# Kernel optimization log

Hardware: AMD Instinct MI355X
Metric: run time of the kernel (lower is better)

## Reference

```python
import jax, jax.numpy as jnp
import numpy as np

N = 100000
D = 128          # atom_input_dim
OUT = 256        # output_dim
HOPS = 3
E = 640000
IN_DIM = D * (HOPS + 1)  # 512


def setup_inputs() -> dict:
    key = jax.random.key(0)
    ks = jax.random.split(key, 16)
    s = 0.02
    inp = {
        "x": jax.random.normal(ks[0], (N, D), dtype=jnp.float32),
        "target": jax.random.randint(ks[1], (E,), 0, HOPS * N, dtype=jnp.int64),
        "src": jax.random.randint(ks[2], (E,), 0, HOPS * N, dtype=jnp.int64),
        "W_in": jax.random.normal(ks[3], (IN_DIM, OUT), dtype=jnp.float32) * s,
        "b_in": jnp.zeros((OUT,), dtype=jnp.float32),
        "W1_0": jax.random.normal(ks[4], (OUT, OUT), dtype=jnp.float32) * s,
        "b1_0": jnp.zeros((OUT,), dtype=jnp.float32),
        "W2_0": jax.random.normal(ks[5], (OUT, OUT), dtype=jnp.float32) * s,
        "b2_0": jnp.zeros((OUT,), dtype=jnp.float32),
        "W1_1": jax.random.normal(ks[6], (OUT, OUT), dtype=jnp.float32) * s,
        "b1_1": jnp.zeros((OUT,), dtype=jnp.float32),
        "W2_1": jax.random.normal(ks[7], (OUT, OUT), dtype=jnp.float32) * s,
        "b2_1": jnp.zeros((OUT,), dtype=jnp.float32),
        "W_skip": jax.random.normal(ks[8], (IN_DIM, OUT), dtype=jnp.float32) * s,
        "b_skip": jnp.zeros((OUT,), dtype=jnp.float32),
    }
    return inp


def reference(x, target, src, W_in, b_in, W1_0, b1_0, W2_0, b2_0,
              W1_1, b1_1, W2_1, b2_1, W_skip, b_skip):
    n = x.shape[0]
    # multi-hop message passing: tile node features HOPS times, gather by src,
    # scatter-add into target over the tiled index space [0, HOPS*n)
    expanded = jnp.tile(x, (HOPS, 1))                       # [HOPS*n, D]
    agg = jnp.zeros_like(expanded).at[target].add(expanded[src])
    # split per-hop chunks and concat with original features -> [n, (HOPS+1)*D]
    feats = jnp.concatenate([x] + [agg[h * n:(h + 1) * n] for h in range(HOPS)], axis=-1)
    h = jax.nn.silu(feats @ W_in + b_in)                    # [n, OUT]
    global_skip = feats @ W_skip + b_skip                   # input_dim != output_dim
    for W1, b1, W2, b2 in ((W1_0, b1_0, W2_0, b2_0), (W1_1, b1_1, W2_1, b2_1)):
        h = (jax.nn.silu(h @ W1 + b1)) @ W2 + b2 + h        # residual MLP block (dropout=0)
    return h + global_skip
```

## Files before the change

kernel.cpp:

```cpp
#include <hip/hip_runtime.h>
#include <math.h>

#define NN 100000
#define DD 128
#define OUT_DIM 256
#define HOPS 3
#define EDGES 640000
#define TGT (HOPS*NN)

typedef short bf16x8 __attribute__((ext_vector_type(8)));
typedef float f32x4 __attribute__((ext_vector_type(4)));

__device__ __forceinline__ unsigned short f2bf(float f) {
    unsigned u = __float_as_uint(f);
    unsigned r = u + 0x7FFFu + ((u >> 16) & 1u);
    return (unsigned short)(r >> 16);
}
__device__ __forceinline__ float bf2f(unsigned short s) {
    return __uint_as_float(((unsigned)s) << 16);
}
__device__ __forceinline__ float silu(float v) { return v / (1.0f + expf(-v)); }

__device__ __forceinline__ int swz(int c, int r) {
    return (c & ~63) | ((c & 63) ^ ((r & 7) << 3));
}

__device__ __forceinline__ void gload16(const unsigned short* g, unsigned short* l) {
    __builtin_amdgcn_global_load_lds(
        (const __attribute__((address_space(1))) void*)g,
        (__attribute__((address_space(3))) void*)l, 16, 0, 0);
}

__global__ __launch_bounds__(256) void k_hist(const int* __restrict__ tgt,
                                              int* __restrict__ cnt) {
    int e = blockIdx.x * 256 + threadIdx.x;
    atomicAdd(&cnt[tgt[e]], 1);
}

__global__ __launch_bounds__(512) void k_scanb(const int* __restrict__ cnt,
                                               int* __restrict__ off,
                                               int* __restrict__ part, int n) {
    __shared__ int s[512];
    int tid = threadIdx.x;
    int g = blockIdx.x * 512 + tid;
    int v = (g < n) ? cnt[g] : 0;
    s[tid] = v;
    __syncthreads();
    for (int d = 1; d < 512; d <<= 1) {
        int a = (tid >= d) ? s[tid - d] : 0;
        __syncthreads();
        s[tid] += a;
        __syncthreads();
    }
    if (g < n) off[g] = s[tid] - v;
    if (tid == 511) part[blockIdx.x] = s[511];
}

__global__ __launch_bounds__(1024) void k_scanp(int* __restrict__ part, int n) {
    __shared__ int s[1024];
    int t = threadIdx.x;
    s[t] = (t < n) ? part[t] : 0;
    __syncthreads();
    for (int d = 1; d < 1024; d <<= 1) {
        int a = (t >= d) ? s[t - d] : 0;
        __syncthreads();
        s[t] += a;
        __syncthreads();
    }
    if (t < n) part[t] = s[t];
}

__global__ __launch_bounds__(512) void k_addoff(int* __restrict__ off,
                                                const int* __restrict__ part,
                                                int* __restrict__ cursor, int n) {
    int g = blockIdx.x * 512 + threadIdx.x;
    if (g >= n) return;
    int add = (blockIdx.x > 0) ? part[blockIdx.x - 1] : 0;
    int o = off[g] + add;
    off[g] = o;
    cursor[g] = o;
}

__global__ __launch_bounds__(256) void k_fill(const int* __restrict__ tgt,
                                              const int* __restrict__ src,
                                              int* __restrict__ cursor,
                                              int* __restrict__ esrc) {
    int e = blockIdx.x * 256 + threadIdx.x;
    int t = tgt[e];
    int p = atomicAdd(&cursor[t], 1);
    esrc[p] = src[e] % NN;
}

__global__ __launch_bounds__(256) void k_aggfeats(const float* __restrict__ x,
                                                  const int* __restrict__ off,
                                                  const int* __restrict__ cur,
                                                  const int* __restrict__ esrc,
                                                  unsigned* __restrict__ feats) {
    int lane = threadIdx.x & 63;
    int r = blockIdx.x * 4 + (threadIdx.x >> 6);
    const float2* x2 = (const float2*)x;
    if (r < NN) {
        float2 v = x2[(size_t)r * 64 + lane];
        int p = lane;
        int ps = (p & ~31) | ((p & 31) ^ ((r & 7) << 2));
        feats[(size_t)r * 256 + ps] =
            (unsigned)f2bf(v.x) | ((unsigned)f2bf(v.y) << 16);
    } else {
        int t = r - NN;
        int hop = t / NN;
        int tn = t - hop * NN;
        int b = off[t], e = cur[t];
        float ax = 0.f, ay = 0.f;
        for (int i = b; i < e; ++i) {
            int sn = esrc[i];
            float2 v = x2[(size_t)sn * 64 + lane];
            ax += v.x; ay += v.y;
        }
        int p = 64 + hop * 64 + lane;
        int ps = (p & ~31) | ((p & 31) ^ ((tn & 7) << 2));
        feats[(size_t)tn * 256 + ps] =
            (unsigned)f2bf(ax) | ((unsigned)f2bf(ay) << 16);
    }
}

__global__ __launch_bounds__(256) void k_wprep(
    const float* __restrict__ Win, const float* __restrict__ Wskip,
    const float* __restrict__ W10, const float* __restrict__ W20,
    const float* __restrict__ W11, const float* __restrict__ W21,
    unsigned short* __restrict__ Wt1, unsigned short* __restrict__ Wt25) {
    int idx = blockIdx.x * 256 + threadIdx.x;
    if (idx < 262144) {
        int c = idx >> 9, k = idx & 511;
        int kl = swz(k, c);
        float v = (c < 256) ? Win[kl * 256 + c] : Wskip[kl * 256 + (c - 256)];
        Wt1[idx] = f2bf(v);
    } else {
        int j = idx - 262144;
        int m = j >> 16, rr = j & 65535;
        int c = rr >> 8, k = rr & 255;
        int kl = swz(k, c);
        const float* Wm = (m == 0) ? W10 : (m == 1) ? W20 : (m == 2) ? W11 : W21;
        Wt25[(size_t)m * 65536 + c * 256 + k] = f2bf(Wm[kl * 256 + c]);
    }
}

template <int K, int EPI>
__global__ __launch_bounds__(256) void k_gemm_t(
    const unsigned short* __restrict__ A, const unsigned short* __restrict__ Wt,
    const float* __restrict__ bias0, const float* __restrict__ bias1,
    const unsigned short* __restrict__ res1, const float* __restrict__ res2,
    unsigned short* __restrict__ Cb, float* __restrict__ Cf) {
    __shared__ unsigned short As[2][128 * 64];
    __shared__ unsigned short Bs[2][128 * 64];

    const int tid = threadIdx.x;
    const int lane = tid & 63;
    const int w = tid >> 6;
    const int row0 = blockIdx.x * 128;
    const int col0 = blockIdx.y * 128;

    const int wr = (w >> 1) * 64;
    const int wc = (w & 1) * 64;
    const int lr = lane & 15;
    const int lk8 = (lane >> 4) * 8;

    f32x4 acc[4][4];
    #pragma unroll
    for (int m = 0; m < 4; ++m)
        #pragma unroll
        for (int n = 0; n < 4; ++n) acc[m][n] = (f32x4){0.f, 0.f, 0.f, 0.f};

    const int NK = K / 64;

    auto STAGE = [&](int buf, int k0) {
        #pragma unroll
        for (int i = 0; i < 4; ++i) {
            int chunk = i * 4 + w;
            int slot = chunk * 64 + lane;
            int r = slot >> 3;
            int kq = (slot & 7) * 8;
            gload16(A + (size_t)(row0 + r) * K + k0 + kq, &As[buf][chunk * 512]);
            gload16(Wt + (size_t)(col0 + r) * K + k0 + kq, &Bs[buf][chunk * 512]);
        }
    };

    STAGE(0, 0);
    asm volatile("s_waitcnt vmcnt(0)" ::: "memory");
    __syncthreads();

    for (int ks = 0; ks < NK; ++ks) {
        int cur = ks & 1;
        if (ks + 1 < NK) STAGE(cur ^ 1, (ks + 1) * 64);

        #pragma unroll
        for (int ks2 = 0; ks2 < 2; ++ks2) {
            bf16x8 af[4], bfr[4];
            #pragma unroll
            for (int m = 0; m < 4; ++m) {
                int row = wr + m * 16 + lr;
                int eo = (ks2 * 32 + lk8) ^ ((row & 7) << 3);
                af[m] = *(const bf16x8*)&As[cur][row * 64 + eo];
            }
            #pragma unroll
            for (int n = 0; n < 4; ++n) {
                int row = wc + n * 16 + lr;
                int eo = (ks2 * 32 + lk8) ^ ((row & 7) << 3);
                bfr[n] = *(const bf16x8*)&Bs[cur][row * 64 + eo];
            }
            #pragma unroll
            for (int m = 0; m < 4; ++m)
                #pragma unroll
                for (int n = 0; n < 4; ++n)
                    acc[m][n] = __builtin_amdgcn_mfma_f32_16x16x32_bf16(
                        af[m], bfr[n], acc[m][n], 0, 0, 0);
        }
        asm volatile("s_waitcnt vmcnt(0)" ::: "memory");
        __syncthreads();
    }

    const int rq = (lane >> 4) * 4;
    #pragma unroll
    for (int m = 0; m < 4; ++m) {
        #pragma unroll
        for (int n = 0; n < 4; ++n) {
            int cg = col0 + wc + n * 16 + lr;
            float bb = (EPI == 3)
                           ? (cg < OUT_DIM ? bias0[cg] : bias1[cg - OUT_DIM])
                           : bias0[cg];
            #pragma unroll
            for (int j = 0; j < 4; ++j) {
                int r = row0 + wr + m * 16 + rq + j;
                if (r >= NN) continue;
                float v = acc[m][n][j] + bb;
                if (EPI == 3) {
                    if (cg < OUT_DIM)
                        Cb[(size_t)r * OUT_DIM + swz(cg, r)] = f2bf(silu(v));
                    else
                        Cf[(size_t)r * OUT_DIM + (cg - OUT_DIM)] = v;
                } else if (EPI == 0) {
                    Cb[(size_t)r * OUT_DIM + swz(cg, r)] = f2bf(silu(v));
                } else if (EPI == 1) {
                    size_t o = (size_t)r * OUT_DIM + swz(cg, r);
                    Cb[o] = f2bf(v + bf2f(res1[o]));
                } else {
                    size_t os = (size_t)r * OUT_DIM + swz(cg, r);
                    size_t ol = (size_t)r * OUT_DIM + cg;
                    Cf[ol] = v + bf2f(res1[os]) + res2[ol];
                }
            }
        }
    }
}

extern "C" void kernel_launch(void* const* d_in, const int* in_sizes, int n_in,
                              void* d_out, int out_size, void* d_ws, size_t ws_size,
                              hipStream_t stream) {
    const float* x      = (const float*)d_in[0];
    const int*   target = (const int*)d_in[1];
    const int*   src    = (const int*)d_in[2];
    const float* W_in   = (const float*)d_in[3];
    const float* b_in   = (const float*)d_in[4];
    const float* W1_0   = (const float*)d_in[5];
    const float* b1_0   = (const float*)d_in[6];
    const float* W2_0   = (const float*)d_in[7];
    const float* b2_0   = (const float*)d_in[8];
    const float* W1_1   = (const float*)d_in[9];
    const float* b1_1   = (const float*)d_in[10];
    const float* W2_1   = (const float*)d_in[11];
    const float* b2_1   = (const float*)d_in[12];
    const float* W_skip = (const float*)d_in[13];
    const float* b_skip = (const float*)d_in[14];
    float* out = (float*)d_out;

    char* p = (char*)d_ws;
    unsigned short* feats = (unsigned short*)p; p += (size_t)NN * 512 * 2;
    unsigned short* h0    = (unsigned short*)p; p += (size_t)NN * 256 * 2;
    unsigned short* h1    = (unsigned short*)p; p += (size_t)NN * 256 * 2;
    unsigned short* tb    = (unsigned short*)p; p += (size_t)NN * 256 * 2;
    unsigned short* Wt1   = (unsigned short*)p; p += 512 * 512 * 2;
    unsigned short* Wt25  = (unsigned short*)p; p += 4 * 256 * 256 * 2;
    int* cnt    = (int*)p; p += (size_t)TGT * 4;
    int* off    = (int*)p; p += (size_t)TGT * 4;
    int* cursor = (int*)p; p += (size_t)TGT * 4;
    int* esrc   = (int*)p; p += (size_t)EDGES * 4;
    int* part   = (int*)p; p += 4096;

    const int SCAN_BLOCKS = (TGT + 511) / 512;

    hipMemsetAsync(cnt, 0, (size_t)TGT * 4, stream);
    k_hist<<<EDGES / 256, 256, 0, stream>>>(target, cnt);
    k_scanb<<<SCAN_BLOCKS, 512, 0, stream>>>(cnt, off, part, TGT);
    k_scanp<<<1, 1024, 0, stream>>>(part, SCAN_BLOCKS);
    k_addoff<<<SCAN_BLOCKS, 512, 0, stream>>>(off, part, cursor, TGT);
    k_fill<<<EDGES / 256, 256, 0, stream>>>(target, src, cursor, esrc);

    k_aggfeats<<<NN, 256, 0, stream>>>(x, off, cursor, esrc, (unsigned*)feats);

    k_wprep<<<2048, 256, 0, stream>>>(W_in, W_skip, W1_0, W2_0, W1_1, W2_1,
                                      Wt1, Wt25);

    const int GM = (NN + 127) / 128;

    k_gemm_t<512, 3><<<dim3(GM, 4), 256, 0, stream>>>(
        feats, Wt1, b_in, b_skip, nullptr, nullptr, h0, out);

    k_gemm_t<256, 0><<<dim3(GM, 2), 256, 0, stream>>>(
        h0, Wt25 + 0 * 65536, b1_0, nullptr, nullptr, nullptr, tb, nullptr);
    k_gemm_t<256, 1><<<dim3(GM, 2), 256, 0, stream>>>(
        tb, Wt25 + 1 * 65536, b2_0, nullptr, h0, nullptr, h1, nullptr);

    k_gemm_t<256, 0><<<dim3(GM, 2), 256, 0, stream>>>(
        h1, Wt25 + 2 * 65536, b1_1, nullptr, nullptr, nullptr, tb, nullptr);
    k_gemm_t<256, 2><<<dim3(GM, 2), 256, 0, stream>>>(
        tb, Wt25 + 3 * 65536, b2_1, nullptr, h1, out, nullptr, out);
}
```

Baseline: 823.3 us.

## Fuse each residual MLP block into one kernel keeping hidden tile in LDS

Replaces the four separate GEMM launches for the two residual MLP blocks with two fused kernels. Each kernel loads a 128-row tile of h into LDS, computes silu(hW1+b1) into the same LDS buffer, then multiplies by W2 and adds the residual, so the intermediate never goes to global memory. The global skip is now stored in bf16 scratch instead of written as fp32 into the output and read back, which lowers skip precision. Blocks of 128 rows give only about 782 blocks of 512 threads and use large LDS, so occupancy may drop.

```diff
diff --git a/kernel.cpp b/kernel.cpp
--- a/kernel.cpp
+++ b/kernel.cpp
@@ -144,12 +144,11 @@
     }
 }
 
-template <int K, int EPI>
-__global__ __launch_bounds__(256) void k_gemm_t(
+__global__ __launch_bounds__(256) void k_gemm1(
     const unsigned short* __restrict__ A, const unsigned short* __restrict__ Wt,
     const float* __restrict__ bias0, const float* __restrict__ bias1,
-    const unsigned short* __restrict__ res1, const float* __restrict__ res2,
-    unsigned short* __restrict__ Cb, float* __restrict__ Cf) {
+    unsigned short* __restrict__ h0, unsigned short* __restrict__ gsk) {
+    const int K = 512;
     __shared__ unsigned short As[2][128 * 64];
     __shared__ unsigned short Bs[2][128 * 64];
 
@@ -169,8 +168,6 @@
     for (int m = 0; m < 4; ++m)
         #pragma unroll
         for (int n = 0; n < 4; ++n) acc[m][n] = (f32x4){0.f, 0.f, 0.f, 0.f};
-
-    const int NK = K / 64;
 
     auto STAGE = [&](int buf, int k0) {
         #pragma unroll
@@ -188,9 +185,9 @@
     asm volatile("s_waitcnt vmcnt(0)" ::: "memory");
     __syncthreads();
 
-    for (int ks = 0; ks < NK; ++ks) {
+    for (int ks = 0; ks < 8; ++ks) {
         int cur = ks & 1;
-        if (ks + 1 < NK) STAGE(cur ^ 1, (ks + 1) * 64);
+        if (ks + 1 < 8) STAGE(cur ^ 1, (ks + 1) * 64);
 
         #pragma unroll
         for (int ks2 = 0; ks2 < 2; ++ks2) {
@@ -224,32 +221,173 @@
         #pragma unroll
         for (int n = 0; n < 4; ++n) {
             int cg = col0 + wc + n * 16 + lr;
-            float bb = (EPI == 3)
-                           ? (cg < OUT_DIM ? bias0[cg] : bias1[cg - OUT_DIM])
-                           : bias0[cg];
+            float bb = (cg < OUT_DIM) ? bias0[cg] : bias1[cg - OUT_DIM];
             #pragma unroll
             for (int j = 0; j < 4; ++j) {
                 int r = row0 + wr + m * 16 + rq + j;
                 if (r >= NN) continue;
                 float v = acc[m][n][j] + bb;
-                if (EPI == 3) {
-                    if (cg < OUT_DIM)
-                        Cb[(size_t)r * OUT_DIM + swz(cg, r)] = f2bf(silu(v));
-                    else
-                        Cf[(size_t)r * OUT_DIM + (cg - OUT_DIM)] = v;
-                } else if (EPI == 0) {
-                    Cb[(size_t)r * OUT_DIM + swz(cg, r)] = f2bf(silu(v));
-                } else if (EPI == 1) {
-                    size_t o = (size_t)r * OUT_DIM + swz(cg, r);
-                    Cb[o] = f2bf(v + bf2f(res1[o]));
+                if (cg < OUT_DIM)
+                    h0[(size_t)r * OUT_DIM + swz(cg, r)] = f2bf(silu(v));
+                else
+                    gsk[(size_t)r * OUT_DIM + (cg - OUT_DIM)] = f2bf(v);
+            }
+        }
+    }
+}
+
+template <int FINAL>
+__global__ __launch_bounds__(512) void k_mlp(
+    const unsigned short* __restrict__ Hin,
+    const unsigned short* __restrict__ W1t, const unsigned short* __restrict__ W2t,
+    const float* __restrict__ b1, const float* __restrict__ b2,
+    const unsigned short* __restrict__ gsk,
+    unsigned short* __restrict__ Hout, float* __restrict__ outf) {
+    __shared__ unsigned short Hs[128 * 256];
+    __shared__ unsigned short Ws[2][256 * 64];
+
+    const int tid = threadIdx.x;
+    const int lane = tid & 63;
+    const int w = tid >> 6;
+    const int wr = (w >> 1) * 32;
+    const int wc = (w & 1) * 128;
+    const int lr = lane & 15;
+    const int lk8 = (lane >> 4) * 8;
+    const int row0 = blockIdx.x * 128;
+
+    auto STAGE_W = [&](const unsigned short* Wt, int buf, int ks) {
+        #pragma unroll
+        for (int i = 0; i < 4; ++i) {
+            int chunk = w * 4 + i;
+            int col = chunk * 8 + (lane >> 3);
+            int ko = ks * 64 + (lane & 7) * 8;
+            gload16(Wt + (size_t)col * 256 + ko, &Ws[buf][chunk * 512]);
+        }
+    };
+
+    #pragma unroll
+    for (int i = 0; i < 8; ++i) {
+        int chunk = w * 8 + i;
+        gload16(Hin + (size_t)row0 * 256 + chunk * 512 + lane * 8,
+                &Hs[chunk * 512]);
+    }
+    STAGE_W(W1t, 0, 0);
+    asm volatile("s_waitcnt vmcnt(0)" ::: "memory");
+    __syncthreads();
+
+    f32x4 acc_t[2][8];
+    #pragma unroll
+    for (int m = 0; m < 2; ++m)
+        #pragma unroll
+        for (int n = 0; n < 8; ++n) acc_t[m][n] = (f32x4){0.f, 0.f, 0.f, 0.f};
+
+    for (int ks = 0; ks < 4; ++ks) {
+        if (ks < 3) STAGE_W(W1t, (ks + 1) & 1, ks + 1);
+        else        STAGE_W(W2t, 0, 0);
+        #pragma unroll
+        for (int ks2 = 0; ks2 < 2; ++ks2) {
+            bf16x8 af[2], bfr[8];
+            #pragma unroll
+            for (int m = 0; m < 2; ++m) {
+                int row = wr + m * 16 + lr;
+                int eo = (ks2 * 32 + lk8) ^ ((row & 7) << 3);
+                af[m] = *(const bf16x8*)&Hs[row * 256 + ks * 64 + eo];
+            }
+            #pragma unroll
+            for (int n = 0; n < 8; ++n) {
+                int col = wc + n * 16 + lr;
+                int eo = (ks2 * 32 + lk8) ^ ((col & 7) << 3);
+                bfr[n] = *(const bf16x8*)&Ws[ks & 1][col * 64 + eo];
+            }
+            #pragma unroll
+            for (int m = 0; m < 2; ++m)
+                #pragma unroll
+                for (int n = 0; n < 8; ++n)
+                    acc_t[m][n] = __builtin_amdgcn_mfma_f32_16x16x32_bf16(
+                        af[m], bfr[n], acc_t[m][n], 0, 0, 0);
+        }
+        asm volatile("s_waitcnt vmcnt(0)" ::: "memory");
+        __syncthreads();
+    }
+
+    const int rq = (lane >> 4) * 4;
+    f32x4 acc2[2][8];
+    #pragma unroll
+    for (int m = 0; m < 2; ++m)
+        #pragma unroll
+        for (int n = 0; n < 8; ++n) {
+            int col = wc + n * 16 + lr;
+            float bb = b2[col];
+            #pragma unroll
+            for (int j = 0; j < 4; ++j) {
+                int row = wr + m * 16 + rq + j;
+                int sc = (col & ~63) | ((col & 63) ^ ((row & 7) << 3));
+                acc2[m][n][j] = bf2f(Hs[row * 256 + sc]) + bb;
+            }
+        }
+    __syncthreads();
+
+    #pragma unroll
+    for (int m = 0; m < 2; ++m)
+        #pragma unroll
+        for (int n = 0; n < 8; ++n) {
+            int col = wc + n * 16 + lr;
+            float bb = b1[col];
+            #pragma unroll
+            for (int j = 0; j < 4; ++j) {
+                int row = wr + m * 16 + rq + j;
+                int sc = (col & ~63) | ((col & 63) ^ ((row & 7) << 3));
+                Hs[row * 256 + sc] = f2bf(silu(acc_t[m][n][j] + bb));
+            }
+        }
+    __syncthreads();
+
+    for (int ks = 0; ks < 4; ++ks) {
+        if (ks < 3) STAGE_W(W2t, (ks + 1) & 1, ks + 1);
+        #pragma unroll
+        for (int ks2 = 0; ks2 < 2; ++ks2) {
+            bf16x8 af[2], bfr[8];
+            #pragma unroll
+            for (int m = 0; m < 2; ++m) {
+                int row = wr + m * 16 + lr;
+                int eo = (ks2 * 32 + lk8) ^ ((row & 7) << 3);
+                af[m] = *(const bf16x8*)&Hs[row * 256 + ks * 64 + eo];
+            }
+            #pragma unroll
+            for (int n = 0; n < 8; ++n) {
+                int col = wc + n * 16 + lr;
+                int eo = (ks2 * 32 + lk8) ^ ((col & 7) << 3);
+                bfr[n] = *(const bf16x8*)&Ws[ks & 1][col * 64 + eo];
+            }
+            #pragma unroll
+            for (int m = 0; m < 2; ++m)
+                #pragma unroll
+                for (int n = 0; n < 8; ++n)
+                    acc2[m][n] = __builtin_amdgcn_mfma_f32_16x16x32_bf16(
+                        af[m], bfr[n], acc2[m][n], 0, 0, 0);
+        }
+        asm volatile("s_waitcnt vmcnt(0)" ::: "memory");
+        __syncthreads();
+    }
+
+    #pragma unroll
+    for (int m = 0; m < 2; ++m)
+        #pragma unroll
+        for (int n = 0; n < 8; ++n) {
+            int col = wc + n * 16 + lr;
+            #pragma unroll
+            for (int j = 0; j < 4; ++j) {
+                int row = wr + m * 16 + rq + j;
+                int r = row0 + row;
+                if (r >= NN) continue;
+                if (FINAL == 0) {
+                    Hout[(size_t)r * 256 + swz(col, row)] = f2bf(acc2[m][n][j]);
                 } else {
-                    size_t os = (size_t)r * OUT_DIM + swz(cg, r);
-                    size_t ol = (size_t)r * OUT_DIM + cg;
-                    Cf[ol] = v + bf2f(res1[os]) + res2[ol];
+                    size_t o = (size_t)r * 256 + col;
+                    outf[o] = acc2[m][n][j] + bf2f(gsk[o]);
                 }
             }
         }
-    }
 }
 
 extern "C" void kernel_launch(void* const* d_in, const int* in_sizes, int n_in,
@@ -276,7 +414,7 @@
     unsigned short* feats = (unsigned short*)p; p += (size_t)NN * 512 * 2;
     unsigned short* h0    = (unsigned short*)p; p += (size_t)NN * 256 * 2;
     unsigned short* h1    = (unsigned short*)p; p += (size_t)NN * 256 * 2;
-    unsigned short* tb    = (unsigned short*)p; p += (size_t)NN * 256 * 2;
+    unsigned short* gsk   = (unsigned short*)p; p += (size_t)NN * 256 * 2;
     unsigned short* Wt1   = (unsigned short*)p; p += 512 * 512 * 2;
     unsigned short* Wt25  = (unsigned short*)p; p += 4 * 256 * 256 * 2;
     int* cnt    = (int*)p; p += (size_t)TGT * 4;
@@ -301,16 +439,10 @@
 
     const int GM = (NN + 127) / 128;
 
-    k_gemm_t<512, 3><<<dim3(GM, 4), 256, 0, stream>>>(
-        feats, Wt1, b_in, b_skip, nullptr, nullptr, h0, out);
-
-    k_gemm_t<256, 0><<<dim3(GM, 2), 256, 0, stream>>>(
-        h0, Wt25 + 0 * 65536, b1_0, nullptr, nullptr, nullptr, tb, nullptr);
-    k_gemm_t<256, 1><<<dim3(GM, 2), 256, 0, stream>>>(
-        tb, Wt25 + 1 * 65536, b2_0, nullptr, h0, nullptr, h1, nullptr);
-
-    k_gemm_t<256, 0><<<dim3(GM, 2), 256, 0, stream>>>(
-        h1, Wt25 + 2 * 65536, b1_1, nullptr, nullptr, nullptr, tb, nullptr);
-    k_gemm_t<256, 2><<<dim3(GM, 2), 256, 0, stream>>>(
-        tb, Wt25 + 3 * 65536, b2_1, nullptr, h1, out, nullptr, out);
-}
+    k_gemm1<<<dim3(GM, 4), 256, 0, stream>>>(feats, Wt1, b_in, b_skip, h0, gsk);
+
+    k_mlp<0><<<GM, 512, 0, stream>>>(h0, Wt25 + 0 * 65536, Wt25 + 1 * 65536,
+                                     b1_0, b2_0, nullptr, h1, nullptr);
+    k_mlp<1><<<GM, 512, 0, stream>>>(h1, Wt25 + 2 * 65536, Wt25 + 3 * 65536,
+                                     b1_1, b2_1, gsk, nullptr, out);
+}
```

Measured after the change: 696.9 us. -15.4%, faster.
